# Performance work log

Hardware: AMD Instinct MI355X
Metric: run time of the kernel (lower is better)

The kernel has to match this reference:

```python
import jax, jax.numpy as jnp
import numpy as np

B, S, E, H = 4, 2048, 1024, 16
D = E // H  # key_size


def setup_inputs() -> dict:
    key = jax.random.key(0)
    ks = jax.random.split(key, 6)
    s = 1.0 / np.sqrt(E)
    return {
        "X": jax.random.normal(ks[0], (B, S, E), dtype=jnp.float32),
        "Wq": jax.random.uniform(ks[1], (E, E), jnp.float32, -s, s),
        "Wk": jax.random.uniform(ks[2], (E, E), jnp.float32, -s, s),
        "Wv": jax.random.uniform(ks[3], (E, E), jnp.float32, -s, s),
        "Wo": jax.random.uniform(ks[4], (E, E), jnp.float32, -s, s),
        "bo": jax.random.uniform(ks[5], (E,), jnp.float32, -s, s),
    }


def reference(X, Wq, Wk, Wv, Wo, bo):
    # Linear layers: y = x @ W^T (torch convention), no bias for q/k/v
    def split(x):  # [B,S,E] -> [B,H,S,D]
        return x.reshape(B, S, H, D).transpose(0, 2, 1, 3)

    q = split(X @ Wq.T)
    k = split(X @ Wk.T)
    v = split(X @ Wv.T)
    scale = jnp.asarray(np.sqrt(D), dtype=X.dtype)
    scores = jnp.einsum("bhqd,bhkd->bhqk", q, k) / scale
    probs = jax.nn.softmax(scores, axis=-1)
    ctx = jnp.einsum("bhqk,bhkd->bhqd", probs, v)
    out = ctx.transpose(0, 2, 1, 3).reshape(B, S, E)
    return out @ Wo.T + bo
```

## Files before the change

### kernel.cpp

```cpp
#include <hip/hip_runtime.h>
#include <hip/hip_bf16.h>

typedef short bf16x8 __attribute__((ext_vector_type(8)));
typedef float f32x4  __attribute__((ext_vector_type(4)));

__device__ __forceinline__ short f2bf(float f) {
    union { float f; unsigned u; } x; x.f = f;
    unsigned r = x.u + 0x7fffu + ((x.u >> 16) & 1u);
    return (short)(r >> 16);
}

__device__ __forceinline__ unsigned bfround(float f) {
    union { float f; unsigned u; } x; x.f = f;
    return x.u + 0x7fffu + ((x.u >> 16) & 1u);
}
__device__ __forceinline__ int pack_bf16(float a, float b) {
    return (int)((bfround(b) & 0xffff0000u) | (bfround(a) >> 16));
}

__device__ __forceinline__ f32x4 mfma32k(bf16x8 a, bf16x8 b, f32x4 c) {
    return __builtin_amdgcn_mfma_f32_16x16x32_bf16(a, b, c, 0, 0, 0);
}

#define GLDS16(g, l)                                                            \
    __builtin_amdgcn_global_load_lds(                                           \
        (const __attribute__((address_space(1))) void*)(g),                     \
        (__attribute__((address_space(3))) void*)(l), 16, 0, 0)

static constexpr int Bb = 4, Ss = 2048, Ee = 1024, Hh = 16, Dd = 64;
static constexpr int Mrows = Bb * Ss;
static constexpr float CL2 = 0.1803368801111204f;

__global__ void cvt_all(const float* __restrict__ X,  const float* __restrict__ Wq,
                        const float* __restrict__ Wk, const float* __restrict__ Wv,
                        const float* __restrict__ Wo,
                        short* __restrict__ Xb, short* __restrict__ Wqk,
                        short* __restrict__ Wvb, short* __restrict__ Wob) {
    int bid = blockIdx.x;
    const float* src; short* dst; int off; float scale = 1.0f;
    if (bid < 8192) {
        src = X; dst = Xb; off = bid * 1024;
    } else {
        int wsel = (bid - 8192) >> 10;
        off = ((bid - 8192) & 1023) * 1024;
        if      (wsel == 0) { src = Wq; dst = Wqk;                scale = CL2; }
        else if (wsel == 1) { src = Wk; dst = Wqk + Ee * Ee; }
        else if (wsel == 2) { src = Wv; dst = Wvb; }
        else                { src = Wo; dst = Wob; }
    }
    int i = off + threadIdx.x * 4;
    float4 v = *(const float4*)(src + i);
    short4 o;
    o.x = f2bf(v.x * scale); o.y = f2bf(v.y * scale);
    o.z = f2bf(v.z * scale); o.w = f2bf(v.w * scale);
    *(short4*)(dst + i) = o;
}

template<bool BIAS_F32OUT, bool PERMC>
__global__ __launch_bounds__(256, 2)
void gemm_bt(const short* __restrict__ A, int lda,
             const short* __restrict__ Bm, int ldb,
             void* __restrict__ C, int ldc,
             const float* __restrict__ bias, int K) {
    __shared__ __align__(16) short sA[128 * 32];
    __shared__ __align__(16) short sB[128 * 32];
    const int t = threadIdx.x, w = t >> 6, l = t & 63;
    const int lane16 = l & 15, quad = l >> 4;
    const int wm = (w >> 1) * 64, wn = (w & 1) * 64;
    const int bm = blockIdx.x, bn = blockIdx.y;

    f32x4 acc[4][4] = {};
    const short* Ab = A + (size_t)bm * 128 * lda;
    const short* Bbp = Bm + (size_t)bn * 128 * ldb;
    const int s0 = w * 64 + l;

    for (int k0 = 0; k0 < K; k0 += 32) {
#pragma unroll
        for (int p = 0; p < 2; ++p) {
            int s = p * 256 + s0;
            int row = s >> 2, cs = s & 3;
            GLDS16(Ab + (size_t)row * lda + k0 + cs * 8, sA + (p * 256 + w * 64) * 8);
            GLDS16(Bbp + (size_t)row * ldb + k0 + cs * 8, sB + (p * 256 + w * 64) * 8);
        }
        __syncthreads();
        bf16x8 af[4], bfr[4];
#pragma unroll
        for (int i = 0; i < 4; ++i) {
            af[i]  = *(const bf16x8*)(sA + (wm + i * 16 + lane16) * 32 + quad * 8);
            bfr[i] = *(const bf16x8*)(sB + (wn + i * 16 + lane16) * 32 + quad * 8);
        }
#pragma unroll
        for (int i = 0; i < 4; ++i)
#pragma unroll
            for (int j = 0; j < 4; ++j)
                acc[i][j] = mfma32k(af[i], bfr[j], acc[i][j]);
        __syncthreads();
    }

    const int sEven = (lane16 >> 2) * 8 + (lane16 & 3);
#pragma unroll
    for (int i = 0; i < 4; ++i)
#pragma unroll
        for (int j = 0; j < 4; ++j) {
            int row = bm * 128 + wm + i * 16 + quad * 4;
            int col = bn * 128 + wn + j * 16 + lane16;
            if (BIAS_F32OUT) {
                float bv = bias[col];
                float* Cf = (float*)C;
#pragma unroll
                for (int r = 0; r < 4; ++r)
                    Cf[(size_t)(row + r) * ldc + col] = acc[i][j][r] + bv;
            } else {
                if (PERMC) col = (col & ~31) | (sEven + (j & 1) * 4);
                short* Cb = (short*)C;
#pragma unroll
                for (int r = 0; r < 4; ++r)
                    Cb[(size_t)(row + r) * ldc + col] = f2bf(acc[i][j][r]);
            }
        }
}

__global__ __launch_bounds__(256, 4)
void attn_kernel(const short* __restrict__ QK, const short* __restrict__ VT,
                 short* __restrict__ CTX) {
    __shared__ __align__(16) short sK[8192];
    __shared__ __align__(16) short sV[8192];
    const int t = threadIdx.x, w = t >> 6, l = t & 63;
    const int lane16 = l & 15, quad = l >> 4;
    const int bh = blockIdx.x, qt = blockIdx.y;
    const int b = bh >> 4, h = bh & 15;

    const short* Qb = QK + ((size_t)(b * 2048 + qt * 128)) * 2048 + h * 64;
    const short* Kb = QK + ((size_t)(b * 2048)) * 2048 + 1024 + h * 64;
    const short* Vb = VT + ((size_t)(h * 64)) * 8192 + (size_t)b * 2048;

#pragma unroll
    for (int p = 0; p < 4; ++p) {
        int c = p * 256 + t;
        int half = c >> 9, row = (c >> 2) & 127, dq = c & 3;
        GLDS16(Qb + (size_t)row * 2048 + half * 32 + dq * 8, sK + (p * 256 + w * 64) * 8);
    }
    __syncthreads();
    bf16x8 qf[2][2];
#pragma unroll
    for (int mt = 0; mt < 2; ++mt)
#pragma unroll
        for (int ks = 0; ks < 2; ++ks)
            qf[mt][ks] = *(const bf16x8*)(sK + ks * 4096 + (w * 32 + mt * 16 + lane16) * 32 + quad * 8);
    __syncthreads();

    float l_i[2] = { 0.0f, 0.0f };
    f32x4 o[2][4] = {};

    for (int kt = 0; kt < 16; ++kt) {
        const short* KbT = Kb + (size_t)kt * 128 * 2048;
        const short* VbT = Vb + kt * 128;
#pragma unroll
        for (int p = 0; p < 4; ++p) {
            int c = p * 256 + t;
            int half = c >> 9, row = (c >> 2) & 127, dq = c & 3;
            GLDS16(KbT + (size_t)row * 2048 + half * 32 + dq * 8, sK + (p * 256 + w * 64) * 8);
        }
#pragma unroll
        for (int p = 0; p < 4; ++p) {
            int c = p * 256 + t;
            int kb = c >> 8, d = (c >> 2) & 63, kq = c & 3;
            GLDS16(VbT + (size_t)d * 8192 + kb * 32 + kq * 8, sV + (p * 256 + w * 64) * 8);
        }
        __syncthreads();

#pragma unroll
        for (int a = 0; a < 4; ++a) {
            f32x4 sc[2][2] = {};
#pragma unroll
            for (int sub = 0; sub < 2; ++sub) {
                int nt = a * 2 + sub;
                bf16x8 kf0 = *(const bf16x8*)(sK + (nt * 16 + lane16) * 32 + quad * 8);
                bf16x8 kf1 = *(const bf16x8*)(sK + 4096 + (nt * 16 + lane16) * 32 + quad * 8);
#pragma unroll
                for (int mt = 0; mt < 2; ++mt) {
                    sc[mt][sub] = mfma32k(kf0, qf[mt][0], sc[mt][sub]);
                    sc[mt][sub] = mfma32k(kf1, qf[mt][1], sc[mt][sub]);
                }
            }
            bf16x8 pf[2];
#pragma unroll
            for (int mt = 0; mt < 2; ++mt) {
                float e0, e1;
                union { int i[4]; bf16x8 v; } u;
#pragma unroll
                for (int sub = 0; sub < 2; ++sub) {
                    e0 = __builtin_amdgcn_exp2f(sc[mt][sub][0]);
                    e1 = __builtin_amdgcn_exp2f(sc[mt][sub][1]);
                    l_i[mt] += e0 + e1;
                    u.i[sub * 2] = pack_bf16(e0, e1);
                    e0 = __builtin_amdgcn_exp2f(sc[mt][sub][2]);
                    e1 = __builtin_amdgcn_exp2f(sc[mt][sub][3]);
                    l_i[mt] += e0 + e1;
                    u.i[sub * 2 + 1] = pack_bf16(e0, e1);
                }
                pf[mt] = u.v;
            }
#pragma unroll
            for (int dt = 0; dt < 4; ++dt) {
                bf16x8 vf = *(const bf16x8*)(sV + a * 2048 + (dt * 16 + lane16) * 32 + quad * 8);
#pragma unroll
                for (int mt = 0; mt < 2; ++mt)
                    o[mt][dt] = mfma32k(pf[mt], vf, o[mt][dt]);
            }
        }
        __syncthreads();
    }

#pragma unroll
    for (int mt = 0; mt < 2; ++mt) {
        l_i[mt] += __shfl_xor(l_i[mt], 16);
        l_i[mt] += __shfl_xor(l_i[mt], 32);
    }
#pragma unroll
    for (int mt = 0; mt < 2; ++mt)
#pragma unroll
        for (int r = 0; r < 4; ++r) {
            float lr = __shfl(l_i[mt], quad * 4 + r);
            float inv = 1.0f / lr;
            int row = b * 2048 + qt * 128 + w * 32 + mt * 16 + quad * 4 + r;
#pragma unroll
            for (int dt = 0; dt < 4; ++dt)
                CTX[(size_t)row * 1024 + h * 64 + dt * 16 + lane16] = f2bf(o[mt][dt][r] * inv);
        }
}

extern "C" void kernel_launch(void* const* d_in, const int* in_sizes, int n_in,
                              void* d_out, int out_size, void* d_ws, size_t ws_size,
                              hipStream_t stream) {
    const float* X  = (const float*)d_in[0];
    const float* Wq = (const float*)d_in[1];
    const float* Wk = (const float*)d_in[2];
    const float* Wv = (const float*)d_in[3];
    const float* Wo = (const float*)d_in[4];
    const float* bo = (const float*)d_in[5];
    float* out = (float*)d_out;

    char* ws = (char*)d_ws;
    constexpr size_t OFF_XB  = 0;
    constexpr size_t OFF_WQK = OFF_XB  + (size_t)Mrows * Ee * 2;
    constexpr size_t OFF_WV  = OFF_WQK + (size_t)2 * Ee * Ee * 2;
    constexpr size_t OFF_WO  = OFF_WV  + (size_t)Ee * Ee * 2;
    constexpr size_t OFF_QK  = OFF_WO  + (size_t)Ee * Ee * 2;
    constexpr size_t OFF_VT  = OFF_QK  + (size_t)Mrows * 2048 * 2;
    constexpr size_t OFF_CTX = OFF_VT  + (size_t)Ee * Mrows * 2;
    short* Xb   = (short*)(ws + OFF_XB);
    short* Wqk  = (short*)(ws + OFF_WQK);
    short* Wvb  = (short*)(ws + OFF_WV);
    short* Wob  = (short*)(ws + OFF_WO);
    short* QKb  = (short*)(ws + OFF_QK);
    short* VTb  = (short*)(ws + OFF_VT);
    short* CTX  = (short*)(ws + OFF_CTX);

    cvt_all<<<12288, 256, 0, stream>>>(X, Wq, Wk, Wv, Wo, Xb, Wqk, Wvb, Wob);

    gemm_bt<false, false><<<dim3(Mrows / 128, 2048 / 128), 256, 0, stream>>>(
        Xb, Ee, Wqk, Ee, QKb, 2048, nullptr, Ee);

    gemm_bt<false, true><<<dim3(Ee / 128, Mrows / 128), 256, 0, stream>>>(
        Wvb, Ee, Xb, Ee, VTb, Mrows, nullptr, Ee);

    attn_kernel<<<dim3(Bb * Hh, Ss / 128), 256, 0, stream>>>(QKb, VTb, CTX);

    gemm_bt<true, false><<<dim3(Mrows / 128, Ee / 128), 256, 0, stream>>>(
        CTX, Ee, Wob, Ee, out, Ee, bo, Ee);
}
```

Before: 273.1 us.

## Double GEMM K-step to 64, simplify bf16 packing, vectorize softmax row-sum accumulation

The GEMM now stages two 32-wide K panels per iteration, so each barrier pair covers twice the MFMA work and the number of synchronizations drops by half, at the cost of twice the LDS per block. In the attention kernel, bf16 packing switches from round-to-nearest-even to round-half-up with a single perm instruction, which cuts ALU work per exponential. The softmax row sums are kept in a 4-wide vector accumulator to break the serial add dependency, and are reduced once at the end.

New measurement: 275.1 us. About the same (+0.8%).

```diff
diff --git a/kernel.cpp b/kernel.cpp
--- a/kernel.cpp
+++ b/kernel.cpp
@@ -10,12 +10,12 @@
     return (short)(r >> 16);
 }
 
-__device__ __forceinline__ unsigned bfround(float f) {
+__device__ __forceinline__ unsigned rbits(float f) {
     union { float f; unsigned u; } x; x.f = f;
-    return x.u + 0x7fffu + ((x.u >> 16) & 1u);
-}
-__device__ __forceinline__ int pack_bf16(float a, float b) {
-    return (int)((bfround(b) & 0xffff0000u) | (bfround(a) >> 16));
+    return x.u + 0x8000u;
+}
+__device__ __forceinline__ int pack2(float a, float b) {
+    return (int)__builtin_amdgcn_perm(rbits(b), rbits(a), 0x07060302u);
 }
 
 __device__ __forceinline__ f32x4 mfma32k(bf16x8 a, bf16x8 b, f32x4 c) {
@@ -62,8 +62,8 @@
              const short* __restrict__ Bm, int ldb,
              void* __restrict__ C, int ldc,
              const float* __restrict__ bias, int K) {
-    __shared__ __align__(16) short sA[128 * 32];
-    __shared__ __align__(16) short sB[128 * 32];
+    __shared__ __align__(16) short sA[2 * 128 * 32];
+    __shared__ __align__(16) short sB[2 * 128 * 32];
     const int t = threadIdx.x, w = t >> 6, l = t & 63;
     const int lane16 = l & 15, quad = l >> 4;
     const int wm = (w >> 1) * 64, wn = (w & 1) * 64;
@@ -72,28 +72,33 @@
     f32x4 acc[4][4] = {};
     const short* Ab = A + (size_t)bm * 128 * lda;
     const short* Bbp = Bm + (size_t)bn * 128 * ldb;
-    const int s0 = w * 64 + l;
-
-    for (int k0 = 0; k0 < K; k0 += 32) {
-#pragma unroll
-        for (int p = 0; p < 2; ++p) {
-            int s = p * 256 + s0;
-            int row = s >> 2, cs = s & 3;
-            GLDS16(Ab + (size_t)row * lda + k0 + cs * 8, sA + (p * 256 + w * 64) * 8);
-            GLDS16(Bbp + (size_t)row * ldb + k0 + cs * 8, sB + (p * 256 + w * 64) * 8);
-        }
-        __syncthreads();
-        bf16x8 af[4], bfr[4];
-#pragma unroll
-        for (int i = 0; i < 4; ++i) {
-            af[i]  = *(const bf16x8*)(sA + (wm + i * 16 + lane16) * 32 + quad * 8);
-            bfr[i] = *(const bf16x8*)(sB + (wn + i * 16 + lane16) * 32 + quad * 8);
-        }
-#pragma unroll
-        for (int i = 0; i < 4; ++i)
-#pragma unroll
-            for (int j = 0; j < 4; ++j)
-                acc[i][j] = mfma32k(af[i], bfr[j], acc[i][j]);
+
+    for (int k0 = 0; k0 < K; k0 += 64) {
+#pragma unroll
+        for (int p = 0; p < 4; ++p) {
+            int c = p * 256 + t;
+            int panel = c >> 9, row = (c >> 2) & 127, cs = c & 3;
+            int col = k0 + panel * 32 + cs * 8;
+            short* ldst = (p * 256 + w * 64) * 8 + (short*)nullptr;
+            GLDS16(Ab + (size_t)row * lda + col, sA + (p * 256 + w * 64) * 8);
+            GLDS16(Bbp + (size_t)row * ldb + col, sB + (p * 256 + w * 64) * 8);
+            (void)ldst;
+        }
+        __syncthreads();
+#pragma unroll
+        for (int s2 = 0; s2 < 2; ++s2) {
+            bf16x8 af[4], bfr[4];
+#pragma unroll
+            for (int i = 0; i < 4; ++i) {
+                af[i]  = *(const bf16x8*)(sA + s2 * 4096 + (wm + i * 16 + lane16) * 32 + quad * 8);
+                bfr[i] = *(const bf16x8*)(sB + s2 * 4096 + (wn + i * 16 + lane16) * 32 + quad * 8);
+            }
+#pragma unroll
+            for (int i = 0; i < 4; ++i)
+#pragma unroll
+                for (int j = 0; j < 4; ++j)
+                    acc[i][j] = mfma32k(af[i], bfr[j], acc[i][j]);
+        }
         __syncthreads();
     }
 
@@ -149,7 +154,7 @@
             qf[mt][ks] = *(const bf16x8*)(sK + ks * 4096 + (w * 32 + mt * 16 + lane16) * 32 + quad * 8);
     __syncthreads();
 
-    float l_i[2] = { 0.0f, 0.0f };
+    f32x4 l4[2] = {};
     f32x4 o[2][4] = {};
 
     for (int kt = 0; kt < 16; ++kt) {
@@ -186,18 +191,16 @@
             bf16x8 pf[2];
 #pragma unroll
             for (int mt = 0; mt < 2; ++mt) {
-                float e0, e1;
                 union { int i[4]; bf16x8 v; } u;
 #pragma unroll
                 for (int sub = 0; sub < 2; ++sub) {
-                    e0 = __builtin_amdgcn_exp2f(sc[mt][sub][0]);
-                    e1 = __builtin_amdgcn_exp2f(sc[mt][sub][1]);
-                    l_i[mt] += e0 + e1;
-                    u.i[sub * 2] = pack_bf16(e0, e1);
-                    e0 = __builtin_amdgcn_exp2f(sc[mt][sub][2]);
-                    e1 = __builtin_amdgcn_exp2f(sc[mt][sub][3]);
-                    l_i[mt] += e0 + e1;
-                    u.i[sub * 2 + 1] = pack_bf16(e0, e1);
+                    f32x4 e;
+#pragma unroll
+                    for (int r = 0; r < 4; ++r)
+                        e[r] = __builtin_amdgcn_exp2f(sc[mt][sub][r]);
+                    l4[mt] += e;
+                    u.i[sub * 2]     = pack2(e[0], e[1]);
+                    u.i[sub * 2 + 1] = pack2(e[2], e[3]);
                 }
                 pf[mt] = u.v;
             }
@@ -212,8 +215,10 @@
         __syncthreads();
     }
 
+    float l_i[2];
 #pragma unroll
     for (int mt = 0; mt < 2; ++mt) {
+        l_i[mt] = (l4[mt][0] + l4[mt][1]) + (l4[mt][2] + l4[mt][3]);
         l_i[mt] += __shfl_xor(l_i[mt], 16);
         l_i[mt] += __shfl_xor(l_i[mt], 32);
     }
```
